# Kernel tuning notes

Hardware: AMD Instinct MI355X
Metric: run time of the kernel (lower is better)

## Reference

```python
import jax, jax.numpy as jnp
import numpy as np

N_BINS = 15  # matches ECELoss(n_bins=15)


def setup_inputs() -> dict:
    key = jax.random.key(0)
    k1, k2 = jax.random.split(key)
    B, C = 2_097_152, 16
    logits = jax.random.normal(k1, (B, C), dtype=jnp.float32) * 2.0
    # binary multi-label targets, stored as float (forward casts to float anyway)
    targets = (jax.random.uniform(k2, (B, C)) < 0.5).astype(jnp.float32)
    return {"logits": logits, "targets": targets}


def reference(logits, targets):
    """Vectorized ECE: single bucketize + segment-sum pass replacing the
    per-class/per-bin Python loops. Same math: for each non-empty (class, bin)
    cell, accumulate |mean_conf - mean_acc| * (cell_count / B), then divide by
    the number of non-empty cells."""
    B, C = logits.shape
    probs = jax.nn.sigmoid(logits)  # [B, C]
    boundaries = jnp.linspace(0.0, 1.0, N_BINS + 1)
    # bin b satisfies boundaries[b] <= p < boundaries[b+1]  (>= start, < end)
    bin_idx = jnp.searchsorted(boundaries, probs, side="right") - 1  # [B, C]
    valid = (bin_idx >= 0) & (bin_idx < N_BINS)  # p == 1.0 falls in no bin
    seg = jnp.where(valid, jnp.arange(C)[None, :] * N_BINS + bin_idx, C * N_BINS)
    seg = seg.reshape(-1)
    num_seg = C * N_BINS + 1  # last segment = dumping ground for invalid
    ones = jnp.ones((B * C,), dtype=probs.dtype)
    cnt = jax.ops.segment_sum(ones, seg, num_segments=num_seg)[:-1]           # [C*n_bins]
    sum_p = jax.ops.segment_sum(probs.reshape(-1), seg, num_segments=num_seg)[:-1]
    sum_t = jax.ops.segment_sum(targets.reshape(-1), seg, num_segments=num_seg)[:-1]
    nonempty = cnt > 0
    safe = jnp.where(nonempty, cnt, 1.0)
    # |avg_confidence - accuracy| * mask.mean()  per non-empty cell
    term = jnp.abs(sum_p / safe - sum_t / safe) * (cnt / B)
    total = jnp.sum(jnp.where(nonempty, term, 0.0))
    count = jnp.sum(nonempty)
    return jnp.where(count > 0, total / count, jnp.zeros((), probs.dtype))
```

## Files before the change

kernel.cpp:

```cpp
#include <hip/hip_runtime.h>
#include <math.h>

#define NC 16
#define NBINS 15
#define NCELL (NC * NBINS)
#define GRID 2048
#define ITERS 64
#define BROWS 2097152.0
#define MAXREP 8

__global__ void __launch_bounds__(256, 8) ece_partial(const float* __restrict__ logits,
                                                      const float* __restrict__ targets,
                                                      float* __restrict__ ws, int nrep) {
    __shared__ unsigned int h[16 * 256];
#pragma unroll
    for (int r = 0; r < 16; ++r) h[r * 256 + threadIdx.x] = 0u;
    __syncthreads();

    const float LOG2E = 1.4426950408889634f;
    const int tid    = blockIdx.x * 256 + threadIdx.x;
    const int stride = GRID * 256;
    const int col    = threadIdx.x;

#define PROC(x, t)                                                        \
    {                                                                     \
        float e = __builtin_amdgcn_exp2f(-(x) * LOG2E);                   \
        float p = __builtin_amdgcn_rcpf(1.0f + e);                        \
        int b = ((int)(p * 15.0f)) & 15;       \
        unsigned int pf = (unsigned int)(p * 1024.0f + 0.5f);             \
        unsigned int val = (1u << 25) | (((unsigned int)(t)) << 18) | pf; \
        atomicAdd(&h[b * 256 + col], val);     \
    }

    for (int k = 0; k < ITERS; k += 4) {
        int i0 = tid + k * stride;
        int i1 = i0 + stride, i2 = i1 + stride, i3 = i2 + stride;
        float l0 = logits[i0], l1 = logits[i1], l2 = logits[i2], l3 = logits[i3];
        float t0 = targets[i0], t1 = targets[i1], t2 = targets[i2], t3 = targets[i3];
        PROC(l0, t0);
        PROC(l1, t1);
        PROC(l2, t2);
        PROC(l3, t3);
    }
#undef PROC
    __syncthreads();

    int idx = threadIdx.x;
    if (idx < NCELL) {
        int cls = idx & 15, bin = idx >> 4;
        int base = bin * 256 + cls;
        unsigned int cnt = 0, tsum = 0, psum = 0;
#pragma unroll
        for (int k = 0; k < 16; ++k) {
            unsigned int v = h[base + 16 * k];
            cnt  += v >> 25;
            tsum += (v >> 18) & 127u;
            psum += v & 0x3FFFFu;
        }
        float* r = ws + (blockIdx.x & (nrep - 1)) * (3 * NCELL);
        atomicAdd(&r[idx],             (float)cnt);
        atomicAdd(&r[NCELL + idx],     (float)psum * (1.0f / 1024.0f));
        atomicAdd(&r[2 * NCELL + idx], (float)tsum);
    }
}

__global__ void __launch_bounds__(256) ece_final(const float* __restrict__ ws,
                                                 float* __restrict__ out, int nrep) {
    __shared__ double s_term[256];
    __shared__ int s_ne[256];
    int i = threadIdx.x;
    double term = 0.0;
    int ne = 0;
    if (i < NCELL) {
        float cnt = 0.0f, sp = 0.0f, st = 0.0f;
        for (int rep = 0; rep < nrep; ++rep) {
            const float* r = ws + rep * (3 * NCELL);
            cnt += r[i];
            sp  += r[NCELL + i];
            st  += r[2 * NCELL + i];
        }
        if (cnt > 0.0f) {
            ne = 1;
            term = fabs((double)sp / (double)cnt - (double)st / (double)cnt) *
                   ((double)cnt / BROWS);
        }
    }
    s_term[i] = term;
    s_ne[i] = ne;
    __syncthreads();
    for (int off = 128; off > 0; off >>= 1) {
        if (i < off) {
            s_term[i] += s_term[i + off];
            s_ne[i]   += s_ne[i + off];
        }
        __syncthreads();
    }
    if (i == 0) out[0] = (s_ne[0] > 0) ? (float)(s_term[0] / (double)s_ne[0]) : 0.0f;
}

extern "C" void kernel_launch(void* const* d_in, const int* in_sizes, int n_in,
                              void* d_out, int out_size, void* d_ws, size_t ws_size,
                              hipStream_t stream) {
    const float* logits  = (const float*)d_in[0];
    const float* targets = (const float*)d_in[1];
    float* ws  = (float*)d_ws;
    float* out = (float*)d_out;

    int nrep = MAXREP;
    while (nrep > 1 && (size_t)(nrep * 3 * NCELL * sizeof(float)) > ws_size) nrep >>= 1;

    hipMemsetAsync(ws, 0, nrep * 3 * NCELL * sizeof(float), stream);
    ece_partial<<<GRID, 256, 0, stream>>>(logits, targets, ws, nrep);
    ece_final<<<1, 256, 0, stream>>>(ws, out, nrep);
}
```

Baseline: 282.8 us.

## Vectorize ECE loads to float4 and widen LDS histogram per lane slot

```diff
diff --git a/kernel.cpp b/kernel.cpp
--- a/kernel.cpp
+++ b/kernel.cpp
@@ -5,54 +5,62 @@
 #define NBINS 15
 #define NCELL (NC * NBINS)
 #define GRID 2048
-#define ITERS 64
+#define VITERS 16
 #define BROWS 2097152.0
 #define MAXREP 8
 
-__global__ void __launch_bounds__(256, 8) ece_partial(const float* __restrict__ logits,
-                                                      const float* __restrict__ targets,
+__device__ __forceinline__ void proc1(float x, float tv, int j, int col,
+                                      unsigned int* h) {
+    const float LOG2E = 1.4426950408889634f;
+    float e = __builtin_amdgcn_exp2f(-x * LOG2E);
+    float p = __builtin_amdgcn_rcpf(1.0f + e);
+    int b = ((int)(p * 15.0f)) & 15;
+    unsigned int u =
+        (unsigned int)(fmaf(tv, 262144.0f, fmaf(p, 1024.0f, 0.5f)));
+    atomicAdd(&h[(b * 4 + j) * 256 + col], u + (1u << 25));
+}
+
+__device__ __forceinline__ void proc4(float4 v, float4 t, int col,
+                                      unsigned int* h) {
+    proc1(v.x, t.x, 0, col, h);
+    proc1(v.y, t.y, 1, col, h);
+    proc1(v.z, t.z, 2, col, h);
+    proc1(v.w, t.w, 3, col, h);
+}
+
+__global__ void __launch_bounds__(256, 2) ece_partial(const float4* __restrict__ logits,
+                                                      const float4* __restrict__ targets,
                                                       float* __restrict__ ws, int nrep) {
-    __shared__ unsigned int h[16 * 256];
+    __shared__ unsigned int h[64 * 256];
 #pragma unroll
-    for (int r = 0; r < 16; ++r) h[r * 256 + threadIdx.x] = 0u;
+    for (int r = 0; r < 64; ++r) h[r * 256 + threadIdx.x] = 0u;
     __syncthreads();
 
-    const float LOG2E = 1.4426950408889634f;
-    const int tid    = blockIdx.x * 256 + threadIdx.x;
-    const int stride = GRID * 256;
-    const int col    = threadIdx.x;
+    const int tid = blockIdx.x * 256 + threadIdx.x;
+    const int S   = GRID * 256;
+    const int col = threadIdx.x;
 
-#define PROC(x, t)                                                        \
-    {                                                                     \
-        float e = __builtin_amdgcn_exp2f(-(x) * LOG2E);                   \
-        float p = __builtin_amdgcn_rcpf(1.0f + e);                        \
-        int b = ((int)(p * 15.0f)) & 15;       \
-        unsigned int pf = (unsigned int)(p * 1024.0f + 0.5f);             \
-        unsigned int val = (1u << 25) | (((unsigned int)(t)) << 18) | pf; \
-        atomicAdd(&h[b * 256 + col], val);     \
+    for (int k = 0; k < VITERS; k += 4) {
+        int i0 = tid + k * S;
+        int i1 = i0 + S, i2 = i1 + S, i3 = i2 + S;
+        float4 a0 = logits[i0], a1 = logits[i1], a2 = logits[i2], a3 = logits[i3];
+        float4 b0 = targets[i0], b1 = targets[i1], b2 = targets[i2], b3 = targets[i3];
+        proc4(a0, b0, col, h);
+        proc4(a1, b1, col, h);
+        proc4(a2, b2, col, h);
+        proc4(a3, b3, col, h);
     }
-
-    for (int k = 0; k < ITERS; k += 4) {
-        int i0 = tid + k * stride;
-        int i1 = i0 + stride, i2 = i1 + stride, i3 = i2 + stride;
-        float l0 = logits[i0], l1 = logits[i1], l2 = logits[i2], l3 = logits[i3];
-        float t0 = targets[i0], t1 = targets[i1], t2 = targets[i2], t3 = targets[i3];
-        PROC(l0, t0);
-        PROC(l1, t1);
-        PROC(l2, t2);
-        PROC(l3, t3);
-    }
-#undef PROC
     __syncthreads();
 
-    int idx = threadIdx.x;
-    if (idx < NCELL) {
-        int cls = idx & 15, bin = idx >> 4;
-        int base = bin * 256 + cls;
+    const int idx = threadIdx.x;
+    const int b = idx >> 4, c = idx & 15;
+    if (b < NBINS) {
+        const int q = c >> 2, j = c & 3;
+        const unsigned int* const row = &h[(b * 4 + j) * 256 + q];
         unsigned int cnt = 0, tsum = 0, psum = 0;
 #pragma unroll
-        for (int k = 0; k < 16; ++k) {
-            unsigned int v = h[base + 16 * k];
+        for (int m = 0; m < 64; ++m) {
+            unsigned int v = row[4 * m];
             cnt  += v >> 25;
             tsum += (v >> 18) & 127u;
             psum += v & 0x3FFFFu;
@@ -101,15 +109,15 @@
 extern "C" void kernel_launch(void* const* d_in, const int* in_sizes, int n_in,
                               void* d_out, int out_size, void* d_ws, size_t ws_size,
                               hipStream_t stream) {
-    const float* logits  = (const float*)d_in[0];
-    const float* targets = (const float*)d_in[1];
+    const float4* logits  = (const float4*)d_in[0];
+    const float4* targets = (const float4*)d_in[1];
     float* ws  = (float*)d_ws;
     float* out = (float*)d_out;
 
     int nrep = MAXREP;
     while (nrep > 1 && (size_t)(nrep * 3 * NCELL * sizeof(float)) > ws_size) nrep >>= 1;
 
-    hipMemsetAsync(ws, 0, nrep * 3 * NCELL * sizeof(float), stream);
+    (void)hipMemsetAsync(ws, 0, nrep * 3 * NCELL * sizeof(float), stream);
     ece_partial<<<GRID, 256, 0, stream>>>(logits, targets, ws, nrep);
     ece_final<<<1, 256, 0, stream>>>(ws, out, nrep);
 }
```

After: 284.9 us. About the same (+0.7%).

## Replace LDS atomic histogram with per-thread register accumulators

Applied to the files above, without the earlier changes.

```diff
diff --git a/kernel.cpp b/kernel.cpp
--- a/kernel.cpp
+++ b/kernel.cpp
@@ -9,40 +9,48 @@
 #define BROWS 2097152.0
 #define MAXREP 8
 
-__global__ void __launch_bounds__(256, 8) ece_partial(const float* __restrict__ logits,
+__global__ void __launch_bounds__(256, 4) ece_partial(const float* __restrict__ logits,
                                                       const float* __restrict__ targets,
                                                       float* __restrict__ ws, int nrep) {
-    __shared__ unsigned int h[16 * 256];
-#pragma unroll
-    for (int r = 0; r < 16; ++r) h[r * 256 + threadIdx.x] = 0u;
-    __syncthreads();
+    __shared__ unsigned int h[NBINS * 256];
 
     const float LOG2E = 1.4426950408889634f;
     const int tid    = blockIdx.x * 256 + threadIdx.x;
     const int stride = GRID * 256;
     const int col    = threadIdx.x;
 
-#define PROC(x, t)                                                        \
-    {                                                                     \
-        float e = __builtin_amdgcn_exp2f(-(x) * LOG2E);                   \
-        float p = __builtin_amdgcn_rcpf(1.0f + e);                        \
-        int b = ((int)(p * 15.0f)) & 15;       \
-        unsigned int pf = (unsigned int)(p * 1024.0f + 0.5f);             \
-        unsigned int val = (1u << 25) | (((unsigned int)(t)) << 18) | pf; \
-        atomicAdd(&h[b * 256 + col], val);     \
+    unsigned int acc[NBINS];
+#pragma unroll
+    for (int b = 0; b < NBINS; ++b) acc[b] = 0u;
+
+    for (int k = 0; k < ITERS; k += 8) {
+        float l[8], t[8];
+#pragma unroll
+        for (int j = 0; j < 8; ++j) {
+            int i = tid + (k + j) * stride;
+            l[j] = logits[i];
+            t[j] = targets[i];
+        }
+        int bs[8];
+        unsigned int us[8];
+#pragma unroll
+        for (int j = 0; j < 8; ++j) {
+            float e = __builtin_amdgcn_exp2f(-l[j] * LOG2E);
+            float p = __builtin_amdgcn_rcpf(1.0f + e);
+            bs[j] = ((int)(p * 15.0f)) & 15;
+            us[j] = (unsigned int)(fmaf(t[j], 262144.0f,
+                                        fmaf(p, 1024.0f, 0.5f))) + (1u << 25);
+        }
+#pragma unroll
+        for (int b = 0; b < NBINS; ++b) {
+#pragma unroll
+            for (int j = 0; j < 8; ++j)
+                acc[b] += (bs[j] == b) ? us[j] : 0u;
+        }
     }
 
-    for (int k = 0; k < ITERS; k += 4) {
-        int i0 = tid + k * stride;
-        int i1 = i0 + stride, i2 = i1 + stride, i3 = i2 + stride;
-        float l0 = logits[i0], l1 = logits[i1], l2 = logits[i2], l3 = logits[i3];
-        float t0 = targets[i0], t1 = targets[i1], t2 = targets[i2], t3 = targets[i3];
-        PROC(l0, t0);
-        PROC(l1, t1);
-        PROC(l2, t2);
-        PROC(l3, t3);
-    }
-#undef PROC
+#pragma unroll
+    for (int b = 0; b < NBINS; ++b) h[b * 256 + col] = acc[b];
     __syncthreads();
 
     int idx = threadIdx.x;
@@ -51,8 +59,8 @@
         int base = bin * 256 + cls;
         unsigned int cnt = 0, tsum = 0, psum = 0;
 #pragma unroll
-        for (int k = 0; k < 16; ++k) {
-            unsigned int v = h[base + 16 * k];
+        for (int kk = 0; kk < 16; ++kk) {
+            unsigned int v = h[base + 16 * kk];
             cnt  += v >> 25;
             tsum += (v >> 18) & 127u;
             psum += v & 0x3FFFFu;
@@ -109,7 +117,7 @@
     int nrep = MAXREP;
     while (nrep > 1 && (size_t)(nrep * 3 * NCELL * sizeof(float)) > ws_size) nrep >>= 1;
 
-    hipMemsetAsync(ws, 0, nrep * 3 * NCELL * sizeof(float), stream);
+    (void)hipMemsetAsync(ws, 0, nrep * 3 * NCELL * sizeof(float), stream);
     ece_partial<<<GRID, 256, 0, stream>>>(logits, targets, ws, nrep);
     ece_final<<<1, 256, 0, stream>>>(ws, out, nrep);
 }
```

Result: no change. 286.0 us (+1.1%).
